# Performance work log

Measured on AMD Instinct MI355X. Metric: run time of the kernel, lower is better.

The kernel has to match this reference:

```python
import jax, jax.numpy as jnp
import numpy as np

# 3 blocks x dilations [1..128] -> 24 residual layers, receptive field ~765
DILATIONS = tuple([1, 2, 4, 8, 16, 32, 64, 128] * 3)
WAVEFORM_BITS = 8


def setup_inputs() -> dict:
    key = jax.random.key(0)
    ks = jax.random.split(key, 8)
    B, C, S, K = 64, 64, 256, 256
    L = len(DILATIONS)
    s = 0.1  # keep gated activations away from saturation
    return {
        "waveform_seed": jax.random.randint(ks[0], (B, 1, 1), 0, K, dtype=jnp.int32),
        "embed": jax.random.normal(ks[1], (K, C), jnp.float32) * s,
        "conv_k": jax.random.normal(ks[2], (L, 2, C, 2 * C), jnp.float32) * s,  # [layer, tap(last/cur), C_in, 2C]
        "conv_b": jnp.zeros((L, 2 * C), jnp.float32),
        "res_w": jax.random.normal(ks[3], (L, C, C), jnp.float32) * s,
        "res_b": jnp.zeros((L, C), jnp.float32),
        "skip_w": jax.random.normal(ks[4], (L, C, S), jnp.float32) * s,
        "skip_b": jnp.zeros((L, S), jnp.float32),
        "out0_w": jax.random.normal(ks[5], (S, K), jnp.float32) * s,
        "out0_b": jnp.zeros((K,), jnp.float32),
        "out1_w": jax.random.normal(ks[6], (K, K), jnp.float32) * s,
        "out1_b": jnp.zeros((K,), jnp.float32),
        "max_infer_samples": 128,
    }


def _generate(seed, embed, conv_k, conv_b, res_w, res_b, skip_w, skip_b,
              out0_w, out0_b, out1_w, out1_b, T):
    B = seed.shape[0]
    C = embed.shape[1]
    sample0 = seed.reshape(B)
    # one circular-buffer queue per layer, length = dilation rate, zero-initialized
    queues0 = tuple(jnp.zeros((d, B, C), embed.dtype) for d in DILATIONS)

    def body(carry, _):
        t, sample, queues = carry
        x_cur = embed[sample]  # [B, C] embedding lookup of previous sample
        skip_sum = jnp.zeros((B, skip_w.shape[-1]), embed.dtype)
        new_queues = []
        for i, d in enumerate(DILATIONS):
            q = queues[i]
            pos = t % d  # circular buffer position == queue pop(0)/append semantics
            x_last = q[pos]
            new_queues.append(q.at[pos].set(x_cur))
            # kernel-size-2 dilated causal conv at a single step == two GEMMs
            h = x_last @ conv_k[i, 0] + x_cur @ conv_k[i, 1] + conv_b[i]  # [B, 2C]
            g = jnp.tanh(h[:, :C]) * jax.nn.sigmoid(h[:, C:])  # gated activation
            x_cur = x_cur + g @ res_w[i] + res_b[i]  # residual out
            skip_sum = skip_sum + g @ skip_w[i] + skip_b[i]  # skip connection
        h0 = jax.nn.relu(skip_sum @ out0_w + out0_b)
        logits = h0 @ out1_w + out1_b  # [B, K]
        nxt = jnp.argmax(logits, axis=-1).astype(jnp.int32)  # deterministic sampling
        return (t + 1, nxt, tuple(new_queues)), (nxt, logits)

    _, (samples, logits) = jax.lax.scan(
        body, (jnp.int32(0), sample0, queues0), None, length=T)
    return samples.transpose(1, 0), logits.transpose(1, 0, 2)  # [B,T], [B,T,K]


def reference(waveform_seed, embed, conv_k, conv_b, res_w, res_b, skip_w, skip_b,
              out0_w, out0_b, out1_w, out1_b, max_infer_samples):
    samples, logits = _generate(waveform_seed, embed, conv_k, conv_b, res_w, res_b,
                                skip_w, skip_b, out0_w, out0_b, out1_w, out1_b,
                                max_infer_samples)
    K = embed.shape[0]
    miu = float(K - 1)
    # rev quantize: map class in [0, 2^bits-1] back to [-1, 1]
    miu_wav = 2.0 * samples.astype(jnp.float32) / (2.0 ** WAVEFORM_BITS - 1.0) - 1.0
    # rev mu-law companding
    pred_wav = jnp.sign(miu_wav) * ((1.0 + miu) ** jnp.abs(miu_wav) - 1.0) / miu
    return pred_wav, logits
```

## Files before the change

kernel.cpp:

```cpp
#include <hip/hip_runtime.h>
#include <math.h>

#define NL 24
#define NB 64
#define TPB 512
#define QROWS 765
#define RING_F  3133440
#define MB_OFF  RING_F
#define CB2_OFF (MB_OFF + 24*64*128)
#define CV_OFF  (CB2_OFF + 24*128)
#define RS_OFF  (CV_OFF + 24*512*48)
#define PH_OFF  (RS_OFF + 24*512*40)

typedef float vf4 __attribute__((ext_vector_type(4)));

struct WBc  { float4 v[12]; };
struct WBrs { float4 v[10]; };

__device__ __forceinline__ float hadd4(float4 v) { return (v.x + v.y) + (v.z + v.w); }
__device__ __forceinline__ void fma4(float4& a, float4 x, float4 w) {
    a.x = fmaf(x.x, w.x, a.x); a.y = fmaf(x.y, w.y, a.y);
    a.z = fmaf(x.z, w.z, a.z); a.w = fmaf(x.w, w.w, a.w);
}
__device__ __forceinline__ void bar() {
    asm volatile("s_waitcnt lgkmcnt(0)" ::: "memory");
    __builtin_amdgcn_s_barrier();
    asm volatile("" ::: "memory");
}
__device__ __forceinline__ void pf_cv(WBc& b, const float4* __restrict__ cvp, int layer, int tid) {
    const float4* p = cvp + (size_t)layer * (12 * 512) + tid;
#pragma unroll
    for (int j = 0; j < 12; ++j) b.v[j] = p[j * 512];
}
__device__ __forceinline__ void pf_rs(WBrs& b, const float4* __restrict__ rsp, int layer, int tid) {
    const float4* p = rsp + (size_t)layer * (10 * 512) + tid;
#pragma unroll
    for (int j = 0; j < 10; ++j) b.v[j] = p[j * 512];
}

__global__ void repack1(const float* __restrict__ conv_k, const float* __restrict__ res_w,
                        const float* __restrict__ conv_b, const float* __restrict__ res_b,
                        float* __restrict__ ws) {
    const int i = blockIdx.x, col = threadIdx.x;
    float* M   = ws + MB_OFF;
    float* cb2 = ws + CB2_OFF;
    if (i == 0) {
        for (int m = 0; m < 64; ++m) M[(size_t)m * 128 + col] = 0.f;
        cb2[col] = conv_b[col];
        return;
    }
    float k1[64];
#pragma unroll
    for (int k = 0; k < 64; ++k)
        k1[k] = conv_k[((size_t)(i * 2 + 1) * 64 + k) * 128 + col];
    for (int m = 0; m < 64; ++m) {
        float a = 0.f;
#pragma unroll
        for (int k = 0; k < 64; ++k)
            a = fmaf(res_w[((size_t)(i - 1) * 64 + m) * 64 + k], k1[k], a);
        M[((size_t)i * 64 + m) * 128 + col] = a;
    }
    float cb = conv_b[i * 128 + col];
#pragma unroll
    for (int k = 0; k < 64; ++k)
        cb = fmaf(res_b[(i - 1) * 64 + k], k1[k], cb);
    cb2[i * 128 + col] = cb;
}

__global__ void repack2(const float* __restrict__ conv_k, const float* __restrict__ res_w,
                        const float* __restrict__ skip_w, const float* __restrict__ out0_w,
                        const float* __restrict__ out1_w, float* __restrict__ ws) {
    const int bb = blockIdx.x, tid = threadIdx.x;
    float4* CV = (float4*)(ws + CV_OFF);
    float4* RS = (float4*)(ws + RS_OFF);
    float4* PH = (float4*)(ws + PH_OFF);
    const float* M = ws + MB_OFF;
    if (bb < NL) {
        const int i = bb, w = tid >> 6, l = tid & 63;
        const int c  = w * 8 + (l & 7);
        const int k0 = (l >> 3) * 8;
        float4* dst = CV + (size_t)i * (12 * 512) + tid;
#pragma unroll
        for (int half = 0; half < 2; ++half) {
            const int cc = c + half * 64;
#pragma unroll
            for (int jj = 0; jj < 2; ++jj) {
                const int kk = k0 + jj * 4;
                float4 a, b, m;
                a.x = conv_k[((size_t)(i * 2 + 0) * 64 + kk + 0) * 128 + cc];
                a.y = conv_k[((size_t)(i * 2 + 0) * 64 + kk + 1) * 128 + cc];
                a.z = conv_k[((size_t)(i * 2 + 0) * 64 + kk + 2) * 128 + cc];
                a.w = conv_k[((size_t)(i * 2 + 0) * 64 + kk + 3) * 128 + cc];
                b.x = conv_k[((size_t)(i * 2 + 1) * 64 + kk + 0) * 128 + cc];
                b.y = conv_k[((size_t)(i * 2 + 1) * 64 + kk + 1) * 128 + cc];
                b.z = conv_k[((size_t)(i * 2 + 1) * 64 + kk + 2) * 128 + cc];
                b.w = conv_k[((size_t)(i * 2 + 1) * 64 + kk + 3) * 128 + cc];
                m.x = M[((size_t)i * 64 + kk + 0) * 128 + cc];
                m.y = M[((size_t)i * 64 + kk + 1) * 128 + cc];
                m.z = M[((size_t)i * 64 + kk + 2) * 128 + cc];
                m.w = M[((size_t)i * 64 + kk + 3) * 128 + cc];
                dst[(half * 6 + 0 + jj) * 512] = a;
                dst[(half * 6 + 2 + jj) * 512] = b;
                dst[(half * 6 + 4 + jj) * 512] = m;
            }
        }
        float4* rdst = RS + (size_t)i * (10 * 512) + tid;
#pragma unroll
        for (int jj = 0; jj < 2; ++jj) {
            float4 v; const int kk = k0 + jj * 4;
            v.x = res_w[((size_t)i * 64 + kk + 0) * 64 + c];
            v.y = res_w[((size_t)i * 64 + kk + 1) * 64 + c];
            v.z = res_w[((size_t)i * 64 + kk + 2) * 64 + c];
            v.w = res_w[((size_t)i * 64 + kk + 3) * 64 + c];
            rdst[jj * 512] = v;
        }
        const int s0 = w * 32 + (l & 15) * 2;
        const int ks = (l >> 4) * 16;
#pragma unroll
        for (int jj = 0; jj < 4; ++jj) {
            float4 v; const int kk = ks + jj * 4;
            v.x = skip_w[((size_t)i * 64 + kk + 0) * 256 + s0];
            v.y = skip_w[((size_t)i * 64 + kk + 1) * 256 + s0];
            v.z = skip_w[((size_t)i * 64 + kk + 2) * 256 + s0];
            v.w = skip_w[((size_t)i * 64 + kk + 3) * 256 + s0];
            rdst[(2 + jj) * 512] = v;
        }
#pragma unroll
        for (int jj = 0; jj < 4; ++jj) {
            float4 v; const int kk = ks + jj * 4; const int s1 = s0 + 1;
            v.x = skip_w[((size_t)i * 64 + kk + 0) * 256 + s1];
            v.y = skip_w[((size_t)i * 64 + kk + 1) * 256 + s1];
            v.z = skip_w[((size_t)i * 64 + kk + 2) * 256 + s1];
            v.w = skip_w[((size_t)i * 64 + kk + 3) * 256 + s1];
            rdst[(6 + jj) * 512] = v;
        }
    } else {
        if (tid >= 64) return;
        const int hb = bb - NL;
        const int which = hb >> 3, w = hb & 7, l = tid;
        const float* W = which ? out1_w : out0_w;
        float4* dst = PH + (size_t)hb * (32 * 64) + l;
        const int c  = w * 32 + (l & 31);
        const int kb = (l >> 5) * 128;
        for (int j = 0; j < 32; ++j) {
            float4 v; const int k0 = kb + j * 4;
            v.x = W[(size_t)(k0 + 0) * 256 + c];
            v.y = W[(size_t)(k0 + 1) * 256 + c];
            v.z = W[(size_t)(k0 + 2) * 256 + c];
            v.w = W[(size_t)(k0 + 3) * 256 + c];
            dst[j * 64] = v;
        }
    }
}

__global__ __launch_bounds__(TPB)
__attribute__((amdgpu_waves_per_eu(2, 2)))
void wavenet_gen(const int* __restrict__ seed,
                 const float* __restrict__ embed,
                 const float* __restrict__ res_b,
                 const float* __restrict__ skip_b,
                 const float* __restrict__ out0_b,
                 const float* __restrict__ out1_b,
                 const int* __restrict__ Tptr,
                 float* __restrict__ out,
                 float* __restrict__ ring,
                 const float4* __restrict__ cvp,
                 const float4* __restrict__ rsp,
                 const float4* __restrict__ php,
                 const float* __restrict__ cb2p)
{
    const int b   = blockIdx.x;
    const int tid = threadIdx.x;
    const int w   = tid >> 6;
    const int l   = tid & 63;
    const int T   = *Tptr;

    __shared__ __align__(16) float xl[2][64];
    __shared__ __align__(16) float yb[2][64];
    __shared__ __align__(16) float gb[2][64];
    __shared__ __align__(16) float skl[256];
    __shared__ __align__(16) float h0l[256];
    __shared__ __align__(16) float ebt[256 * 64];
    __shared__ __align__(16) float cb2S[NL * 128];
    __shared__ __align__(16) float rbS[NL * 64];
    __shared__ __align__(16) float o0bS[256], o1bS[256], sbtS[256];
    __shared__ float wmaxv[8];
    __shared__ int   wmaxi[8];

    float* q = ring + (size_t)b * (QROWS * 64);

    {
        vf4* q4 = (vf4*)q;
        const vf4 z = (vf4){0.f, 0.f, 0.f, 0.f};
        for (int idx = tid; idx < QROWS * 64 / 4; idx += TPB)
            __builtin_nontemporal_store(z, &q4[idx]);
        const float4* s4; float4* d4;
        s4 = (const float4*)embed;  d4 = (float4*)ebt;
        for (int idx = tid; idx < 256 * 64 / 4; idx += TPB) d4[idx] = s4[idx];
        s4 = (const float4*)cb2p;   d4 = (float4*)cb2S;
        for (int idx = tid; idx < NL * 128 / 4; idx += TPB) d4[idx] = s4[idx];
        s4 = (const float4*)res_b;  d4 = (float4*)rbS;
        for (int idx = tid; idx < NL * 64 / 4; idx += TPB) d4[idx] = s4[idx];
        s4 = (const float4*)out0_b; d4 = (float4*)o0bS;
        for (int idx = tid; idx < 64; idx += TPB) d4[idx] = s4[idx];
        s4 = (const float4*)out1_b; d4 = (float4*)o1bS;
        for (int idx = tid; idx < 64; idx += TPB) d4[idx] = s4[idx];
        if (tid < 256) {
            float acc = 0.f;
            for (int i = 0; i < NL; ++i) acc += skip_b[i * 256 + tid];
            sbtS[tid] = acc;
        }
    }
    __syncthreads();
    if (tid < 64) {
        const int smp = seed[b];
        yb[0][tid] = ebt[smp * 64 + tid];
        yb[1][tid] = 0.f;
        xl[0][tid] = 0.f;
        xl[1][tid] = 0.f;
        gb[0][tid] = 0.f;
        gb[1][tid] = 0.f;
    }
    __syncthreads();

    WBc  CVa, CVb;
    WBrs RS;
    pf_cv(CVa, cvp, 0, tid);

    float* out_pred = out + (size_t)b * T;
    float* out_log  = out + (size_t)NB * T + (size_t)b * T * 256;

    const int c   = w * 8 + (l & 7);
    const int k0  = (l >> 3) * 8;
    const int ks  = (l >> 4) * 16;
    const int s0  = w * 32 + (l & 15) * 2;
    const int c2  = w * 32 + (l & 31);
    const int kb2 = (l >> 5) * 128;

    float skv0 = 0.f, skv1 = 0.f;

    for (int t = 0; t < T; ++t) {

        auto phase = [&](WBc& cur, WBc& nxt, const int i) {
            const int j = (i + 1 < NL) ? (i + 1) : 0;
            float xln = 0.f;
            if (w == 7) {
                const int dj = 1 << (j & 7);
                const int s  = (i == NL - 1) ? (t + 1) : t;
                const int row = 255 * (j >> 3) + (dj - 1) + (s & (dj - 1));
                xln = __builtin_nontemporal_load(&q[(size_t)row * 64 + l]);
            }
            if (i) pf_rs(RS, rsp, i - 1, tid);
            pf_cv(nxt, cvp, j, tid);
            if (w == 6 && i) {
                const int dp = 1 << ((i - 1) & 7);
                const int row = 255 * ((i - 1) >> 3) + (dp - 1) + (t & (dp - 1));
                __builtin_nontemporal_store(yb[(i - 1) & 1][l], &q[(size_t)row * 64 + l]);
            }
            const int ybi = i ? ((i - 1) & 1) : 0;
            const int gbi = (i - 1) & 1;
            const float4 xl0 = *(const float4*)&xl[i & 1][k0];
            const float4 xl1 = *(const float4*)&xl[i & 1][k0 + 4];
            const float4 yp0 = *(const float4*)&yb[ybi][k0];
            const float4 yp1 = *(const float4*)&yb[ybi][k0 + 4];
            const float4 gp0 = *(const float4*)&gb[gbi][k0];
            const float4 gp1 = *(const float4*)&gb[gbi][k0 + 4];
            float4 aA = make_float4(0.f, 0.f, 0.f, 0.f);
            float4 aB = make_float4(0.f, 0.f, 0.f, 0.f);
            fma4(aA, xl0, cur.v[0]); fma4(aA, xl1, cur.v[1]);
            fma4(aA, yp0, cur.v[2]); fma4(aA, yp1, cur.v[3]);
            fma4(aA, gp0, cur.v[4]); fma4(aA, gp1, cur.v[5]);
            fma4(aB, xl0, cur.v[6]); fma4(aB, xl1, cur.v[7]);
            fma4(aB, yp0, cur.v[8]); fma4(aB, yp1, cur.v[9]);
            fma4(aB, gp0, cur.v[10]); fma4(aB, gp1, cur.v[11]);
            float hA = hadd4(aA), hB = hadd4(aB);
            hA += __shfl_xor(hA, 8);  hB += __shfl_xor(hB, 8);
            hA += __shfl_xor(hA, 16); hB += __shfl_xor(hB, 16);
            hA += __shfl_xor(hA, 32); hB += __shfl_xor(hB, 32);
            hA += cb2S[i * 128 + c];
            hB += cb2S[i * 128 + 64 + c];
            const float g = tanhf(hA) * (1.f / (1.f + expf(-hB)));
            float ynew = 0.f;
            if (i) {
                float4 ra = make_float4(0.f, 0.f, 0.f, 0.f);
                fma4(ra, gp0, RS.v[0]); fma4(ra, gp1, RS.v[1]);
                float racc = hadd4(ra);
                racc += __shfl_xor(racc, 8);
                racc += __shfl_xor(racc, 16);
                racc += __shfl_xor(racc, 32);
                ynew = yb[ybi][c] + racc + rbS[(i - 1) * 64 + c];
                const float4 gs0 = *(const float4*)&gb[gbi][ks];
                const float4 gs1 = *(const float4*)&gb[gbi][ks + 4];
                const float4 gs2 = *(const float4*)&gb[gbi][ks + 8];
                const float4 gs3 = *(const float4*)&gb[gbi][ks + 12];
                float4 sa0 = make_float4(0.f, 0.f, 0.f, 0.f);
                float4 sa1 = make_float4(0.f, 0.f, 0.f, 0.f);
                fma4(sa0, gs0, RS.v[2]); fma4(sa0, gs1, RS.v[3]);
                fma4(sa0, gs2, RS.v[4]); fma4(sa0, gs3, RS.v[5]);
                fma4(sa1, gs0, RS.v[6]); fma4(sa1, gs1, RS.v[7]);
                fma4(sa1, gs2, RS.v[8]); fma4(sa1, gs3, RS.v[9]);
                float ss0 = hadd4(sa0), ss1 = hadd4(sa1);
                ss0 += __shfl_xor(ss0, 16); ss1 += __shfl_xor(ss1, 16);
                ss0 += __shfl_xor(ss0, 32); ss1 += __shfl_xor(ss1, 32);
                skv0 += ss0;
                skv1 += ss1;
            }
            if (l < 8) gb[i & 1][w * 8 + l] = g;
            if (i && l < 8) yb[i & 1][w * 8 + l] = ynew;
            if (w == 7) xl[j & 1][l] = xln;
            bar();
        };

#pragma unroll 1
        for (int ii = 0; ii < NL; ii += 2) {
            phase(CVa, CVb, ii);
            phase(CVb, CVa, ii + 1);
        }

        {
            pf_rs(RS, rsp, NL - 1, tid);
            const float4 gs0 = *(const float4*)&gb[1][ks];
            const float4 gs1 = *(const float4*)&gb[1][ks + 4];
            const float4 gs2 = *(const float4*)&gb[1][ks + 8];
            const float4 gs3 = *(const float4*)&gb[1][ks + 12];
            float4 sa0 = make_float4(0.f, 0.f, 0.f, 0.f);
            float4 sa1 = make_float4(0.f, 0.f, 0.f, 0.f);
            fma4(sa0, gs0, RS.v[2]); fma4(sa0, gs1, RS.v[3]);
            fma4(sa0, gs2, RS.v[4]); fma4(sa0, gs3, RS.v[5]);
            fma4(sa1, gs0, RS.v[6]); fma4(sa1, gs1, RS.v[7]);
            fma4(sa1, gs2, RS.v[8]); fma4(sa1, gs3, RS.v[9]);
            float ss0 = hadd4(sa0), ss1 = hadd4(sa1);
            ss0 += __shfl_xor(ss0, 16); ss1 += __shfl_xor(ss1, 16);
            ss0 += __shfl_xor(ss0, 32); ss1 += __shfl_xor(ss1, 32);
            skv0 += ss0;
            skv1 += ss1;
            if (l < 16) {
                skl[s0] = skv0 + sbtS[s0];
                skl[s0 + 1] = skv1 + sbtS[s0 + 1];
            }
            skv0 = 0.f; skv1 = 0.f;
            if (w == 6) {
                const int row = 510 + 127 + (t & 127);
                __builtin_nontemporal_store(yb[1][l], &q[(size_t)row * 64 + l]);
            }
            bar();
        }
        {
            const float4* hp = php + ((size_t)w * 32) * 64 + l;
            float4 ha = make_float4(0.f, 0.f, 0.f, 0.f);
#pragma unroll 8
            for (int cc = 0; cc < 32; ++cc) {
                float4 wv = hp[cc * 64];
                float4 sv = *(const float4*)&skl[kb2 + cc * 4];
                fma4(ha, sv, wv);
            }
            float hs = hadd4(ha);
            hs += __shfl_xor(hs, 32);
            const float h0 = fmaxf(hs + o0bS[c2], 0.f);
            if (l < 32) h0l[c2] = h0;
        }
        bar();
        {
            const float4* hp = php + ((size_t)(8 + w) * 32) * 64 + l;
            float4 la = make_float4(0.f, 0.f, 0.f, 0.f);
#pragma unroll 8
            for (int cc = 0; cc < 32; ++cc) {
                float4 wv = hp[cc * 64];
                float4 hv = *(const float4*)&h0l[kb2 + cc * 4];
                fma4(la, hv, wv);
            }
            float ls = hadd4(la);
            ls += __shfl_xor(ls, 32);
            const float logit = ls + o1bS[c2];
            if (l < 32)
                __builtin_nontemporal_store(logit, &out_log[(size_t)t * 256 + c2]);
            float bv = logit; int bi = c2;
#pragma unroll
            for (int off = 1; off <= 16; off <<= 1) {
                const float ov = __shfl_xor(bv, off);
                const int   oi = __shfl_xor(bi, off);
                if (ov > bv || (ov == bv && oi < bi)) { bv = ov; bi = oi; }
            }
            if (l == 0) { wmaxv[w] = bv; wmaxi[w] = bi; }
        }
        bar();
        {
            float fv = wmaxv[0]; int fi = wmaxi[0];
#pragma unroll
            for (int ww = 1; ww < 8; ++ww) {
                const float vv = wmaxv[ww]; const int vi = wmaxi[ww];
                if (vv > fv || (vv == fv && vi < fi)) { fv = vv; fi = vi; }
            }
            if (tid < 64) yb[0][tid] = ebt[fi * 64 + tid];
            if (tid == 0) {
                const float mw = (float)fi * (2.0f / 255.0f) - 1.0f;
                const float a  = fabsf(mw);
                const float p  = (exp2f(8.0f * a) - 1.0f) * (1.0f / 255.0f);
                __builtin_nontemporal_store((mw < 0.f) ? -p : p, &out_pred[t]);
            }
        }
        bar();
    }
}

extern "C" void kernel_launch(void* const* d_in, const int* in_sizes, int n_in,
                              void* d_out, int out_size, void* d_ws, size_t ws_size,
                              hipStream_t stream) {
    const int*   seed   = (const int*)  d_in[0];
    const float* embed  = (const float*)d_in[1];
    const float* conv_k = (const float*)d_in[2];
    const float* conv_b = (const float*)d_in[3];
    const float* res_w  = (const float*)d_in[4];
    const float* res_b  = (const float*)d_in[5];
    const float* skip_w = (const float*)d_in[6];
    const float* skip_b = (const float*)d_in[7];
    const float* out0_w = (const float*)d_in[8];
    const float* out0_b = (const float*)d_in[9];
    const float* out1_w = (const float*)d_in[10];
    const float* out1_b = (const float*)d_in[11];
    const int*   Tptr   = (const int*)  d_in[12];

    float* ws = (float*)d_ws;
    float* ring = ws;
    const float4* cvp  = (const float4*)(ws + CV_OFF);
    const float4* rsp  = (const float4*)(ws + RS_OFF);
    const float4* php  = (const float4*)(ws + PH_OFF);
    const float*  cb2p = ws + CB2_OFF;

    repack1<<<dim3(NL), dim3(128), 0, stream>>>(conv_k, res_w, conv_b, res_b, ws);
    repack2<<<dim3(NL + 16), dim3(512), 0, stream>>>(conv_k, res_w, skip_w, out0_w, out1_w, ws);

    wavenet_gen<<<dim3(NB), dim3(TPB), 0, stream>>>(
        seed, embed, res_b, skip_b, out0_b, out1_b, Tptr,
        (float*)d_out, ring, cvp, rsp, php, cb2p);
}
```

Measured before the change: 7.906 ms.

## Double threads per block to 1024 and halve per-thread weight registers

Each per-batch block now runs 1024 threads instead of 512, so every thread holds half as many prefetched weight float4s for the conv, residual/skip and output GEMVs. The repacked weight layouts and all index mappings are rewritten for the new thread split, and reductions now use intra-quad or intra-16 lane shuffles. The waves-per-EU attribute is removed. The aim is to shorten the serial per-step latency by spreading each layer's dot products over more lanes. The cost is more waves taking part in every barrier and more shuffle steps.

```diff
diff --git a/kernel.cpp b/kernel.cpp
--- a/kernel.cpp
+++ b/kernel.cpp
@@ -3,19 +3,19 @@
 
 #define NL 24
 #define NB 64
-#define TPB 512
+#define TPB 1024
 #define QROWS 765
 #define RING_F  3133440
 #define MB_OFF  RING_F
 #define CB2_OFF (MB_OFF + 24*64*128)
 #define CV_OFF  (CB2_OFF + 24*128)
-#define RS_OFF  (CV_OFF + 24*512*48)
-#define PH_OFF  (RS_OFF + 24*512*40)
+#define RS_OFF  (CV_OFF + 24*6*1024*4)
+#define PH_OFF  (RS_OFF + 24*5*1024*4)
 
 typedef float vf4 __attribute__((ext_vector_type(4)));
 
-struct WBc  { float4 v[12]; };
-struct WBrs { float4 v[10]; };
+struct WBc  { float4 v[6]; };
+struct WBrs { float4 v[5]; };
 
 __device__ __forceinline__ float hadd4(float4 v) { return (v.x + v.y) + (v.z + v.w); }
 __device__ __forceinline__ void fma4(float4& a, float4 x, float4 w) {
@@ -28,14 +28,14 @@
     asm volatile("" ::: "memory");
 }
 __device__ __forceinline__ void pf_cv(WBc& b, const float4* __restrict__ cvp, int layer, int tid) {
-    const float4* p = cvp + (size_t)layer * (12 * 512) + tid;
-#pragma unroll
-    for (int j = 0; j < 12; ++j) b.v[j] = p[j * 512];
+    const float4* p = cvp + (size_t)layer * (6 * 1024) + tid;
+#pragma unroll
+    for (int j = 0; j < 6; ++j) b.v[j] = p[j * 1024];
 }
 __device__ __forceinline__ void pf_rs(WBrs& b, const float4* __restrict__ rsp, int layer, int tid) {
-    const float4* p = rsp + (size_t)layer * (10 * 512) + tid;
-#pragma unroll
-    for (int j = 0; j < 10; ++j) b.v[j] = p[j * 512];
+    const float4* p = rsp + (size_t)layer * (5 * 1024) + tid;
+#pragma unroll
+    for (int j = 0; j < 5; ++j) b.v[j] = p[j * 1024];
 }
 
 __global__ void repack1(const float* __restrict__ conv_k, const float* __restrict__ res_w,
@@ -76,85 +76,68 @@
     float4* PH = (float4*)(ws + PH_OFF);
     const float* M = ws + MB_OFF;
     if (bb < NL) {
-        const int i = bb, w = tid >> 6, l = tid & 63;
-        const int c  = w * 8 + (l & 7);
-        const int k0 = (l >> 3) * 8;
-        float4* dst = CV + (size_t)i * (12 * 512) + tid;
+        const int i  = bb;
+        const int p  = tid >> 4;
+        const int kk = (tid & 15) * 4;
+        float4* dst = CV + (size_t)i * (6 * 1024) + tid;
 #pragma unroll
         for (int half = 0; half < 2; ++half) {
-            const int cc = c + half * 64;
-#pragma unroll
-            for (int jj = 0; jj < 2; ++jj) {
-                const int kk = k0 + jj * 4;
-                float4 a, b, m;
-                a.x = conv_k[((size_t)(i * 2 + 0) * 64 + kk + 0) * 128 + cc];
-                a.y = conv_k[((size_t)(i * 2 + 0) * 64 + kk + 1) * 128 + cc];
-                a.z = conv_k[((size_t)(i * 2 + 0) * 64 + kk + 2) * 128 + cc];
-                a.w = conv_k[((size_t)(i * 2 + 0) * 64 + kk + 3) * 128 + cc];
-                b.x = conv_k[((size_t)(i * 2 + 1) * 64 + kk + 0) * 128 + cc];
-                b.y = conv_k[((size_t)(i * 2 + 1) * 64 + kk + 1) * 128 + cc];
-                b.z = conv_k[((size_t)(i * 2 + 1) * 64 + kk + 2) * 128 + cc];
-                b.w = conv_k[((size_t)(i * 2 + 1) * 64 + kk + 3) * 128 + cc];
-                m.x = M[((size_t)i * 64 + kk + 0) * 128 + cc];
-                m.y = M[((size_t)i * 64 + kk + 1) * 128 + cc];
-                m.z = M[((size_t)i * 64 + kk + 2) * 128 + cc];
-                m.w = M[((size_t)i * 64 + kk + 3) * 128 + cc];
-                dst[(half * 6 + 0 + jj) * 512] = a;
-                dst[(half * 6 + 2 + jj) * 512] = b;
-                dst[(half * 6 + 4 + jj) * 512] = m;
-            }
-        }
-        float4* rdst = RS + (size_t)i * (10 * 512) + tid;
-#pragma unroll
-        for (int jj = 0; jj < 2; ++jj) {
-            float4 v; const int kk = k0 + jj * 4;
-            v.x = res_w[((size_t)i * 64 + kk + 0) * 64 + c];
-            v.y = res_w[((size_t)i * 64 + kk + 1) * 64 + c];
-            v.z = res_w[((size_t)i * 64 + kk + 2) * 64 + c];
-            v.w = res_w[((size_t)i * 64 + kk + 3) * 64 + c];
-            rdst[jj * 512] = v;
-        }
-        const int s0 = w * 32 + (l & 15) * 2;
-        const int ks = (l >> 4) * 16;
+            const int cc = p + half * 64;
+            float4 a, b, m;
+            a.x = conv_k[((size_t)(i * 2 + 0) * 64 + kk + 0) * 128 + cc];
+            a.y = conv_k[((size_t)(i * 2 + 0) * 64 + kk + 1) * 128 + cc];
+            a.z = conv_k[((size_t)(i * 2 + 0) * 64 + kk + 2) * 128 + cc];
+            a.w = conv_k[((size_t)(i * 2 + 0) * 64 + kk + 3) * 128 + cc];
+            b.x = conv_k[((size_t)(i * 2 + 1) * 64 + kk + 0) * 128 + cc];
+            b.y = conv_k[((size_t)(i * 2 + 1) * 64 + kk + 1) * 128 + cc];
+            b.z = conv_k[((size_t)(i * 2 + 1) * 64 + kk + 2) * 128 + cc];
+            b.w = conv_k[((size_t)(i * 2 + 1) * 64 + kk + 3) * 128 + cc];
+            m.x = M[((size_t)i * 64 + kk + 0) * 128 + cc];
+            m.y = M[((size_t)i * 64 + kk + 1) * 128 + cc];
+            m.z = M[((size_t)i * 64 + kk + 2) * 128 + cc];
+            m.w = M[((size_t)i * 64 + kk + 3) * 128 + cc];
+            dst[(0 + half) * 1024] = a;
+            dst[(2 + half) * 1024] = b;
+            dst[(4 + half) * 1024] = m;
+        }
+        float4* rdst = RS + (size_t)i * (5 * 1024) + tid;
+        {
+            float4 v;
+            v.x = res_w[((size_t)i * 64 + kk + 0) * 64 + p];
+            v.y = res_w[((size_t)i * 64 + kk + 1) * 64 + p];
+            v.z = res_w[((size_t)i * 64 + kk + 2) * 64 + p];
+            v.w = res_w[((size_t)i * 64 + kk + 3) * 64 + p];
+            rdst[0] = v;
+        }
+        const int s  = tid >> 2;
+        const int ks = (tid & 3) * 16;
 #pragma unroll
         for (int jj = 0; jj < 4; ++jj) {
-            float4 v; const int kk = ks + jj * 4;
-            v.x = skip_w[((size_t)i * 64 + kk + 0) * 256 + s0];
-            v.y = skip_w[((size_t)i * 64 + kk + 1) * 256 + s0];
-            v.z = skip_w[((size_t)i * 64 + kk + 2) * 256 + s0];
-            v.w = skip_w[((size_t)i * 64 + kk + 3) * 256 + s0];
-            rdst[(2 + jj) * 512] = v;
-        }
-#pragma unroll
-        for (int jj = 0; jj < 4; ++jj) {
-            float4 v; const int kk = ks + jj * 4; const int s1 = s0 + 1;
-            v.x = skip_w[((size_t)i * 64 + kk + 0) * 256 + s1];
-            v.y = skip_w[((size_t)i * 64 + kk + 1) * 256 + s1];
-            v.z = skip_w[((size_t)i * 64 + kk + 2) * 256 + s1];
-            v.w = skip_w[((size_t)i * 64 + kk + 3) * 256 + s1];
-            rdst[(6 + jj) * 512] = v;
+            float4 v; const int k0 = ks + jj * 4;
+            v.x = skip_w[((size_t)i * 64 + k0 + 0) * 256 + s];
+            v.y = skip_w[((size_t)i * 64 + k0 + 1) * 256 + s];
+            v.z = skip_w[((size_t)i * 64 + k0 + 2) * 256 + s];
+            v.w = skip_w[((size_t)i * 64 + k0 + 3) * 256 + s];
+            rdst[(1 + jj) * 1024] = v;
         }
     } else {
-        if (tid >= 64) return;
-        const int hb = bb - NL;
-        const int which = hb >> 3, w = hb & 7, l = tid;
+        const int which = bb - NL;
         const float* W = which ? out1_w : out0_w;
-        float4* dst = PH + (size_t)hb * (32 * 64) + l;
-        const int c  = w * 32 + (l & 31);
-        const int kb = (l >> 5) * 128;
-        for (int j = 0; j < 32; ++j) {
+        float4* dst = PH + (size_t)which * (16 * 1024) + tid;
+        const int c2 = tid >> 2;
+        const int kb = (tid & 3) * 64;
+        for (int j = 0; j < 16; ++j) {
             float4 v; const int k0 = kb + j * 4;
-            v.x = W[(size_t)(k0 + 0) * 256 + c];
-            v.y = W[(size_t)(k0 + 1) * 256 + c];
-            v.z = W[(size_t)(k0 + 2) * 256 + c];
-            v.w = W[(size_t)(k0 + 3) * 256 + c];
-            dst[j * 64] = v;
+            v.x = W[(size_t)(k0 + 0) * 256 + c2];
+            v.y = W[(size_t)(k0 + 1) * 256 + c2];
+            v.z = W[(size_t)(k0 + 2) * 256 + c2];
+            v.w = W[(size_t)(k0 + 3) * 256 + c2];
+            dst[j * 1024] = v;
         }
     }
 }
 
 __global__ __launch_bounds__(TPB)
-__attribute__((amdgpu_waves_per_eu(2, 2)))
 void wavenet_gen(const int* __restrict__ seed,
                  const float* __restrict__ embed,
                  const float* __restrict__ res_b,
@@ -184,8 +167,8 @@
     __shared__ __align__(16) float cb2S[NL * 128];
     __shared__ __align__(16) float rbS[NL * 64];
     __shared__ __align__(16) float o0bS[256], o1bS[256], sbtS[256];
-    __shared__ float wmaxv[8];
-    __shared__ int   wmaxi[8];
+    __shared__ float wmaxv[16];
+    __shared__ int   wmaxi[16];
 
     float* q = ring + (size_t)b * (QROWS * 64);
 
@@ -230,84 +213,76 @@
     float* out_pred = out + (size_t)b * T;
     float* out_log  = out + (size_t)NB * T + (size_t)b * T * 256;
 
-    const int c   = w * 8 + (l & 7);
-    const int k0  = (l >> 3) * 8;
-    const int ks  = (l >> 4) * 16;
-    const int s0  = w * 32 + (l & 15) * 2;
-    const int c2  = w * 32 + (l & 31);
-    const int kb2 = (l >> 5) * 128;
-
-    float skv0 = 0.f, skv1 = 0.f;
+    const int p   = tid >> 4;
+    const int kk  = (tid & 15) * 4;
+    const int s   = tid >> 2;
+    const int ks  = (tid & 3) * 16;
+    const int kb2 = (tid & 3) * 64;
+
+    float skv = 0.f;
 
     for (int t = 0; t < T; ++t) {
 
         auto phase = [&](WBc& cur, WBc& nxt, const int i) {
             const int j = (i + 1 < NL) ? (i + 1) : 0;
             float xln = 0.f;
-            if (w == 7) {
+            if (w == 15) {
                 const int dj = 1 << (j & 7);
-                const int s  = (i == NL - 1) ? (t + 1) : t;
-                const int row = 255 * (j >> 3) + (dj - 1) + (s & (dj - 1));
+                const int st = (i == NL - 1) ? (t + 1) : t;
+                const int row = 255 * (j >> 3) + (dj - 1) + (st & (dj - 1));
                 xln = __builtin_nontemporal_load(&q[(size_t)row * 64 + l]);
             }
             if (i) pf_rs(RS, rsp, i - 1, tid);
             pf_cv(nxt, cvp, j, tid);
-            if (w == 6 && i) {
+            if (w == 14 && i) {
                 const int dp = 1 << ((i - 1) & 7);
                 const int row = 255 * ((i - 1) >> 3) + (dp - 1) + (t & (dp - 1));
                 __builtin_nontemporal_store(yb[(i - 1) & 1][l], &q[(size_t)row * 64 + l]);
             }
             const int ybi = i ? ((i - 1) & 1) : 0;
             const int gbi = (i - 1) & 1;
-            const float4 xl0 = *(const float4*)&xl[i & 1][k0];
-            const float4 xl1 = *(const float4*)&xl[i & 1][k0 + 4];
-            const float4 yp0 = *(const float4*)&yb[ybi][k0];
-            const float4 yp1 = *(const float4*)&yb[ybi][k0 + 4];
-            const float4 gp0 = *(const float4*)&gb[gbi][k0];
-            const float4 gp1 = *(const float4*)&gb[gbi][k0 + 4];
+            const float4 xlv = *(const float4*)&xl[i & 1][kk];
+            const float4 ypv = *(const float4*)&yb[ybi][kk];
+            const float4 gpv = *(const float4*)&gb[gbi][kk];
             float4 aA = make_float4(0.f, 0.f, 0.f, 0.f);
             float4 aB = make_float4(0.f, 0.f, 0.f, 0.f);
-            fma4(aA, xl0, cur.v[0]); fma4(aA, xl1, cur.v[1]);
-            fma4(aA, yp0, cur.v[2]); fma4(aA, yp1, cur.v[3]);
-            fma4(aA, gp0, cur.v[4]); fma4(aA, gp1, cur.v[5]);
-            fma4(aB, xl0, cur.v[6]); fma4(aB, xl1, cur.v[7]);
-            fma4(aB, yp0, cur.v[8]); fma4(aB, yp1, cur.v[9]);
-            fma4(aB, gp0, cur.v[10]); fma4(aB, gp1, cur.v[11]);
+            fma4(aA, xlv, cur.v[0]); fma4(aA, ypv, cur.v[2]); fma4(aA, gpv, cur.v[4]);
+            fma4(aB, xlv, cur.v[1]); fma4(aB, ypv, cur.v[3]); fma4(aB, gpv, cur.v[5]);
             float hA = hadd4(aA), hB = hadd4(aB);
+            hA += __shfl_xor(hA, 1);  hB += __shfl_xor(hB, 1);
+            hA += __shfl_xor(hA, 2);  hB += __shfl_xor(hB, 2);
+            hA += __shfl_xor(hA, 4);  hB += __shfl_xor(hB, 4);
             hA += __shfl_xor(hA, 8);  hB += __shfl_xor(hB, 8);
-            hA += __shfl_xor(hA, 16); hB += __shfl_xor(hB, 16);
-            hA += __shfl_xor(hA, 32); hB += __shfl_xor(hB, 32);
-            hA += cb2S[i * 128 + c];
-            hB += cb2S[i * 128 + 64 + c];
+            hA += cb2S[i * 128 + p];
+            hB += cb2S[i * 128 + 64 + p];
             const float g = tanhf(hA) * (1.f / (1.f + expf(-hB)));
             float ynew = 0.f;
             if (i) {
                 float4 ra = make_float4(0.f, 0.f, 0.f, 0.f);
-                fma4(ra, gp0, RS.v[0]); fma4(ra, gp1, RS.v[1]);
+                fma4(ra, gpv, RS.v[0]);
                 float racc = hadd4(ra);
+                racc += __shfl_xor(racc, 1);
+                racc += __shfl_xor(racc, 2);
+                racc += __shfl_xor(racc, 4);
                 racc += __shfl_xor(racc, 8);
-                racc += __shfl_xor(racc, 16);
-                racc += __shfl_xor(racc, 32);
-                ynew = yb[ybi][c] + racc + rbS[(i - 1) * 64 + c];
+                ynew = yb[ybi][p] + racc + rbS[(i - 1) * 64 + p];
                 const float4 gs0 = *(const float4*)&gb[gbi][ks];
                 const float4 gs1 = *(const float4*)&gb[gbi][ks + 4];
                 const float4 gs2 = *(const float4*)&gb[gbi][ks + 8];
                 const float4 gs3 = *(const float4*)&gb[gbi][ks + 12];
-                float4 sa0 = make_float4(0.f, 0.f, 0.f, 0.f);
-                float4 sa1 = make_float4(0.f, 0.f, 0.f, 0.f);
-                fma4(sa0, gs0, RS.v[2]); fma4(sa0, gs1, RS.v[3]);
-                fma4(sa0, gs2, RS.v[4]); fma4(sa0, gs3, RS.v[5]);
-                fma4(sa1, gs0, RS.v[6]); fma4(sa1, gs1, RS.v[7]);
-                fma4(sa1, gs2, RS.v[8]); fma4(sa1, gs3, RS.v[9]);
-                float ss0 = hadd4(sa0), ss1 = hadd4(sa1);
-                ss0 += __shfl_xor(ss0, 16); ss1 += __shfl_xor(ss1, 16);
-                ss0 += __shfl_xor(ss0, 32); ss1 += __shfl_xor(ss1, 32);
-                skv0 += ss0;
-                skv1 += ss1;
-            }
-            if (l < 8) gb[i & 1][w * 8 + l] = g;
-            if (i && l < 8) yb[i & 1][w * 8 + l] = ynew;
-            if (w == 7) xl[j & 1][l] = xln;
+                float4 sa = make_float4(0.f, 0.f, 0.f, 0.f);
+                fma4(sa, gs0, RS.v[1]); fma4(sa, gs1, RS.v[2]);
+                fma4(sa, gs2, RS.v[3]); fma4(sa, gs3, RS.v[4]);
+                float ss = hadd4(sa);
+                ss += __shfl_xor(ss, 1);
+                ss += __shfl_xor(ss, 2);
+                skv += ss;
+            }
+            if ((tid & 15) == 0) {
+                gb[i & 1][p] = g;
+                if (i) yb[i & 1][p] = ynew;
+            }
+            if (w == 15) xl[j & 1][l] = xln;
             bar();
         };
 
@@ -323,60 +298,55 @@
             const float4 gs1 = *(const float4*)&gb[1][ks + 4];
             const float4 gs2 = *(const float4*)&gb[1][ks + 8];
             const float4 gs3 = *(const float4*)&gb[1][ks + 12];
-            float4 sa0 = make_float4(0.f, 0.f, 0.f, 0.f);
-            float4 sa1 = make_float4(0.f, 0.f, 0.f, 0.f);
-            fma4(sa0, gs0, RS.v[2]); fma4(sa0, gs1, RS.v[3]);
-            fma4(sa0, gs2, RS.v[4]); fma4(sa0, gs3, RS.v[5]);
-            fma4(sa1, gs0, RS.v[6]); fma4(sa1, gs1, RS.v[7]);
-            fma4(sa1, gs2, RS.v[8]); fma4(sa1, gs3, RS.v[9]);
-            float ss0 = hadd4(sa0), ss1 = hadd4(sa1);
-            ss0 += __shfl_xor(ss0, 16); ss1 += __shfl_xor(ss1, 16);
-            ss0 += __shfl_xor(ss0, 32); ss1 += __shfl_xor(ss1, 32);
-            skv0 += ss0;
-            skv1 += ss1;
-            if (l < 16) {
-                skl[s0] = skv0 + sbtS[s0];
-                skl[s0 + 1] = skv1 + sbtS[s0 + 1];
-            }
-            skv0 = 0.f; skv1 = 0.f;
-            if (w == 6) {
+            float4 sa = make_float4(0.f, 0.f, 0.f, 0.f);
+            fma4(sa, gs0, RS.v[1]); fma4(sa, gs1, RS.v[2]);
+            fma4(sa, gs2, RS.v[3]); fma4(sa, gs3, RS.v[4]);
+            float ss = hadd4(sa);
+            ss += __shfl_xor(ss, 1);
+            ss += __shfl_xor(ss, 2);
+            skv += ss;
+            if ((tid & 3) == 0) skl[s] = skv + sbtS[s];
+            skv = 0.f;
+            if (w == 14) {
                 const int row = 510 + 127 + (t & 127);
                 __builtin_nontemporal_store(yb[1][l], &q[(size_t)row * 64 + l]);
             }
             bar();
         }
         {
-            const float4* hp = php + ((size_t)w * 32) * 64 + l;
+            const float4* hp = php + tid;
             float4 ha = make_float4(0.f, 0.f, 0.f, 0.f);
-#pragma unroll 8
-            for (int cc = 0; cc < 32; ++cc) {
-                float4 wv = hp[cc * 64];
-                float4 sv = *(const float4*)&skl[kb2 + cc * 4];
+#pragma unroll
+            for (int jj = 0; jj < 16; ++jj) {
+                const float4 wv = hp[jj * 1024];
+                const float4 sv = *(const float4*)&skl[kb2 + jj * 4];
                 fma4(ha, sv, wv);
             }
             float hs = hadd4(ha);
-            hs += __shfl_xor(hs, 32);
-            const float h0 = fmaxf(hs + o0bS[c2], 0.f);
-            if (l < 32) h0l[c2] = h0;
+            hs += __shfl_xor(hs, 1);
+            hs += __shfl_xor(hs, 2);
+            const float h0 = fmaxf(hs + o0bS[s], 0.f);
+            if ((tid & 3) == 0) h0l[s] = h0;
         }
         bar();
         {
-            const float4* hp = php + ((size_t)(8 + w) * 32) * 64 + l;
+            const float4* hp = php + (16 * 1024) + tid;
             float4 la = make_float4(0.f, 0.f, 0.f, 0.f);
-#pragma unroll 8
-            for (int cc = 0; cc < 32; ++cc) {
-                float4 wv = hp[cc * 64];
-                float4 hv = *(const float4*)&h0l[kb2 + cc * 4];
+#pragma unroll
+            for (int jj = 0; jj < 16; ++jj) {
+                const float4 wv = hp[jj * 1024];
+                const float4 hv = *(const float4*)&h0l[kb2 + jj * 4];
                 fma4(la, hv, wv);
             }
             float ls = hadd4(la);
-            ls += __shfl_xor(ls, 32);
-            const float logit = ls + o1bS[c2];
-            if (l < 32)
-                __builtin_nontemporal_store(logit, &out_log[(size_t)t * 256 + c2]);
-            float bv = logit; int bi = c2;
-#pragma unroll
-            for (int off = 1; off <= 16; off <<= 1) {
+            ls += __shfl_xor(ls, 1);
+            ls += __shfl_xor(ls, 2);
+            const float logit = ls + o1bS[s];
+            if ((tid & 3) == 0)
+                __builtin_nontemporal_store(logit, &out_log[(size_t)t * 256 + s]);
+            float bv = logit; int bi = s;
+#pragma unroll
+            for (int off = 1; off <= 32; off <<= 1) {
                 const float ov = __shfl_xor(bv, off);
                 const int   oi = __shfl_xor(bi, off);
                 if (ov > bv || (ov == bv && oi < bi)) { bv = ov; bi = oi; }
@@ -387,7 +357,7 @@
         {
             float fv = wmaxv[0]; int fi = wmaxi[0];
 #pragma unroll
-            for (int ww = 1; ww < 8; ++ww) {
+            for (int ww = 1; ww < 16; ++ww) {
                 const float vv = wmaxv[ww]; const int vi = wmaxi[ww];
                 if (vv > fv || (vv == fv && vi < fi)) { fv = vv; fi = vi; }
             }
@@ -395,8 +365,8 @@
             if (tid == 0) {
                 const float mw = (float)fi * (2.0f / 255.0f) - 1.0f;
                 const float a  = fabsf(mw);
-                const float p  = (exp2f(8.0f * a) - 1.0f) * (1.0f / 255.0f);
-                __builtin_nontemporal_store((mw < 0.f) ? -p : p, &out_pred[t]);
+                const float pp = (exp2f(8.0f * a) - 1.0f) * (1.0f / 255.0f);
+                __builtin_nontemporal_store((mw < 0.f) ? -pp : pp, &out_pred[t]);
             }
         }
         bar();
@@ -428,7 +398,7 @@
     const float*  cb2p = ws + CB2_OFF;
 
     repack1<<<dim3(NL), dim3(128), 0, stream>>>(conv_k, res_w, conv_b, res_b, ws);
-    repack2<<<dim3(NL + 16), dim3(512), 0, stream>>>(conv_k, res_w, skip_w, out0_w, out1_w, ws);
+    repack2<<<dim3(NL + 2), dim3(1024), 0, stream>>>(conv_k, res_w, skip_w, out0_w, out1_w, ws);
 
     wavenet_gen<<<dim3(NB), dim3(TPB), 0, stream>>>(
         seed, embed, res_b, skip_b, out0_b, out1_b, Tptr,
```

Result: slower. 9.089 ms (+15.0%).
